# Kernel tuning notes

Hardware: AMD Instinct MI355X
Metric: run time of the kernel (lower is better)

## Reference

```python
import jax, jax.numpy as jnp
import numpy as np

EPROJS = 1024
DUNITS = 1024
AHEADS = 4
DK = 512
DV = 512
ACONV_CHANS = 128
ACONV_FILTS = 100
B = 16
T = 2048


def setup_inputs() -> dict:
    key = jax.random.key(0)
    ks = jax.random.split(key, 16)
    s = 0.02
    inp = {}
    inp["enc_hs_pad"] = jax.random.normal(ks[0], (B, T, EPROJS), jnp.float32)
    # lengths in [T//2, T] so no batch element is fully padded
    inp["enc_hs_len"] = jnp.sort(jax.random.randint(ks[1], (B,), T // 2, T + 1))
    inp["dec_z"] = jax.random.normal(ks[2], (B, DUNITS), jnp.float32)
    # per-head parameters, stacked on leading head axis where shapes match
    inp["Wq"] = jax.random.normal(ks[3], (AHEADS, DK, DUNITS), jnp.float32) * s
    inp["bq"] = jnp.zeros((AHEADS, DK), jnp.float32)
    inp["Wk"] = jax.random.normal(ks[4], (AHEADS, DK, EPROJS), jnp.float32) * s
    inp["Wv"] = jax.random.normal(ks[5], (AHEADS, DV, EPROJS), jnp.float32) * s
    inp["g_w"] = jax.random.normal(ks[6], (AHEADS, DK), jnp.float32) * s
    inp["g_b"] = jnp.zeros((AHEADS,), jnp.float32)
    inp["Watt"] = jax.random.normal(ks[7], (AHEADS, DK, ACONV_CHANS), jnp.float32) * s
    # conv kernels have DIFFERENT widths per head: 2*afilts+1, afilts = ACONV_FILTS*(h+1)//AHEADS
    for h in range(AHEADS):
        af = ACONV_FILTS * (h + 1) // AHEADS
        inp[f"conv_w_{h}"] = jax.random.normal(ks[8 + h], (ACONV_CHANS, 1, 2 * af + 1), jnp.float32) * s
    inp["Wo"] = jax.random.normal(ks[12], (EPROJS, AHEADS * DV), jnp.float32) * s
    return inp


def reference(enc_hs_pad, enc_hs_len, dec_z, Wq, bq, Wk, Wv, g_w, g_b, Watt,
              conv_w_0, conv_w_1, conv_w_2, conv_w_3, Wo):
    conv_ws = [conv_w_0, conv_w_1, conv_w_2, conv_w_3]
    Bb, Tt, _ = enc_hs_pad.shape
    scaling = jnp.float32(1.0) / jnp.sqrt(jnp.float32(DK))
    pos = jnp.arange(Tt)[None, :]                                   # (1,T)
    pad_mask = pos >= enc_hs_len[:, None]                           # (B,T) True at padding
    # att_prev=None path: uniform attention over valid frames (same for all heads)
    att_prev = (~pad_mask).astype(jnp.float32) / enc_hs_len[:, None].astype(jnp.float32)

    K = jnp.einsum('bte,hke->hbtk', enc_hs_pad, Wk)                 # pre_compute_k
    V = jnp.einsum('bte,hve->hbtv', enc_hs_pad, Wv)                 # pre_compute_v
    Q = jnp.einsum('bd,hkd->hbk', dec_z, Wq) + bq[:, None, :]       # mlp_q per head

    x = att_prev[:, None, :]                                        # (B,1,T) NCH
    cs, ws = [], []
    for h in range(AHEADS):  # heads have distinct conv widths -> structural loop
        wk = conv_ws[h]                                             # (C,1,2*af+1)
        af = (wk.shape[-1] - 1) // 2
        conv = jax.lax.conv_general_dilated(
            x, wk, window_strides=(1,), padding=[(af, af)],
            dimension_numbers=('NCH', 'OIH', 'NCH'))                # (B,C,T)
        att_feat = jnp.einsum('bct,kc->btk', conv, Watt[h])         # mlp_att
        e = jnp.einsum('btk,k->bt', jnp.tanh(K[h] + att_feat + Q[h][:, None, :]), g_w[h]) + g_b[h]
        e = jnp.where(pad_mask, -jnp.inf, e)
        w = jax.nn.softmax(scaling * e, axis=1)                     # (B,T)
        ws.append(w)
        cs.append(jnp.einsum('btv,bt->bv', V[h], w))                # weighted sum
    c = jnp.concatenate(cs, axis=1) @ Wo.T                          # (B,eprojs)
    return c, jnp.stack(ws)                                         # (B,eprojs), (H,B,T)
```

## Files before the change

### kernel.cpp

```cpp
#include <hip/hip_runtime.h>

#define EPROJS 1024
#define DUNITS 1024
#define AHEADS 4
#define DK 512
#define DV 512
#define CCH 128
#define BB 16
#define TT 2048

typedef __attribute__((ext_vector_type(8))) short bf16x8;
typedef __attribute__((ext_vector_type(4))) float f32x4;

static __device__ __forceinline__ short f2bf(float x) {
  unsigned u = __float_as_uint(x);
  unsigned r = u + 0x7fffu + ((u >> 16) & 1u);
  return (short)(r >> 16);
}
static __device__ __forceinline__ float bf2f(short x) {
  return __uint_as_float(((unsigned)(unsigned short)x) << 16);
}

static __device__ __forceinline__ float fast_tanh(float x) {
  float e2 = __expf(2.0f * x);
  return 1.0f - 2.0f / (e2 + 1.0f);
}

__global__ __launch_bounds__(256) void cvt_kernel(const float* __restrict__ in,
                                                  short* __restrict__ out, int n4) {
  int i = blockIdx.x * blockDim.x + threadIdx.x;
  if (i >= n4) return;
  float4 v = reinterpret_cast<const float4*>(in)[i];
  short4 o;
  o.x = f2bf(v.x); o.y = f2bf(v.y); o.z = f2bf(v.z); o.w = f2bf(v.w);
  reinterpret_cast<short4*>(out)[i] = o;
}

__global__ __launch_bounds__(256) void packB_kernel(const float* __restrict__ Wk,
                                                    const float* __restrict__ Watt,
                                                    short* __restrict__ Bp) {
  int idx = blockIdx.x * 256 + threadIdx.x;
  if (idx >= 294912) return;
  int lane = idx & 63; int t = idx >> 6;
  int nblk = t & 31; t >>= 5;
  int kkidx = t % 36; int h = t / 36;
  int col = nblk * 16 + (lane & 15);
  int k0 = kkidx * 32 + (lane >> 4) * 8;
  const float* src;
  if (k0 < 1024) src = Wk + ((size_t)(h * DK + col)) * EPROJS + k0;
  else           src = Watt + ((size_t)(h * DK + col)) * CCH + (k0 - 1024);
  float4 v0 = reinterpret_cast<const float4*>(src)[0];
  float4 v1 = reinterpret_cast<const float4*>(src)[1];
  short o[8] = { f2bf(v0.x), f2bf(v0.y), f2bf(v0.z), f2bf(v0.w),
                 f2bf(v1.x), f2bf(v1.y), f2bf(v1.z), f2bf(v1.w) };
  *reinterpret_cast<bf16x8*>(Bp + (size_t)idx * 8) = *reinterpret_cast<bf16x8*>(o);
}

__global__ __launch_bounds__(128) void prefix_kernel(const float* __restrict__ w0,
                                                     const float* __restrict__ w1,
                                                     const float* __restrict__ w2,
                                                     const float* __restrict__ w3,
                                                     float* __restrict__ S) {
  int h = blockIdx.x, c = threadIdx.x;
  const float* wk = (h == 0) ? w0 : (h == 1) ? w1 : (h == 2) ? w2 : w3;
  int af = (100 * (h + 1)) >> 2;
  int L = 2 * af + 1;
  float* Sh = S + h * 202 * 128;
  float s = 0.f;
  Sh[c] = 0.f;
  for (int t = 0; t < L; ++t) { s += wk[c * L + t]; Sh[(t + 1) * 128 + c] = s; }
}

__global__ __launch_bounds__(256) void q_kernel(const float* __restrict__ dec,
                                                const float* __restrict__ Wq,
                                                const float* __restrict__ bq,
                                                float* __restrict__ Qb) {
  int wid = (blockIdx.x * blockDim.x + threadIdx.x) >> 6;
  int lane = threadIdx.x & 63;
  int k = wid & (DK - 1); int hb = wid >> 9; int b = hb & (BB - 1); int h = hb >> 4;
  const float4* d4 = reinterpret_cast<const float4*>(dec + b * DUNITS);
  const float4* w4 = reinterpret_cast<const float4*>(Wq + (size_t)(h * DK + k) * DUNITS);
  float s = 0.f;
#pragma unroll
  for (int j = 0; j < 4; ++j) {
    float4 a = d4[j * 64 + lane], w = w4[j * 64 + lane];
    s += a.x * w.x + a.y * w.y + a.z * w.z + a.w * w.w;
  }
#pragma unroll
  for (int off = 32; off; off >>= 1) s += __shfl_xor(s, off);
  if (lane == 0) Qb[wid] = s + bq[h * DK + k];
}

__global__ __launch_bounds__(512, 3) void e_kernel(const short* __restrict__ encb,
                                                   const short* __restrict__ Bp,
                                                   const float* __restrict__ S,
                                                   const float* __restrict__ Qb,
                                                   const float* __restrict__ gw,
                                                   const float* __restrict__ gb,
                                                   const int* __restrict__ lens,
                                                   float* __restrict__ ebuf) {
  __shared__ short At[2][64 * 128];
  __shared__ short Ac[64 * 128];
  __shared__ float epart[8][64];

  int bid = blockIdx.x;
  int h = bid >> 9; int rem = bid & 511; int b = rem >> 5; int t0 = (rem & 31) << 6;
  int tid = threadIdx.x; int w = tid >> 6; int l = tid & 63;
  int lrow = l & 15, lhi = l >> 4;
  int len = lens[b];
  float invlen = 1.0f / (float)len;
  int af = (100 * (h + 1)) >> 2;

  const short* encB = encb + ((size_t)(b * TT + t0)) * EPROJS;
  const short* BpH = Bp + (size_t)h * 36 * 32 * 64 * 8;

  int srow = tid >> 3;
  int sc = tid & 7;
  int wo0 = srow * 128 + ((sc ^ (srow & 7)) << 3);
  int wo1 = srow * 128 + (((sc + 8) ^ (srow & 7)) << 3);
  const short* sbase = encB + (size_t)srow * EPROJS + sc * 8;

  int rx = lrow & 7;

  bf16x8 s0 = *reinterpret_cast<const bf16x8*>(sbase);
  bf16x8 s1 = *reinterpret_cast<const bf16x8*>(sbase + 64);

  const float* Sh = S + h * 202 * 128;
  for (int idx = tid; idx < 64 * 128; idx += 512) {
    int r = idx >> 7, c = idx & 127;
    int t = t0 + r;
    int lo = af - t; if (lo < 0) lo = 0;
    int hi = af - t + len - 1; if (hi > 2 * af) hi = 2 * af;
    float v = 0.f;
    if (hi >= lo) v = (Sh[(hi + 1) * 128 + c] - Sh[lo * 128 + c]) * invlen;
    Ac[r * 128 + (((c >> 3) ^ (r & 7)) << 3) + (c & 7)] = f2bf(v);
  }

  f32x4 acc[4][4] = {};

  bf16x8 bnext[4];
#pragma unroll
  for (int n = 0; n < 4; ++n)
    bnext[n] = *reinterpret_cast<const bf16x8*>(BpH + (((size_t)32 * 32 + (w * 4 + n)) * 64 + l) * 8);

  __syncthreads();

#pragma unroll
  for (int kk = 0; kk < 4; ++kk) {
    bf16x8 bcur[4];
#pragma unroll
    for (int n = 0; n < 4; ++n) bcur[n] = bnext[n];
    int nk = (kk < 3) ? (33 + kk) : 0;
#pragma unroll
    for (int n = 0; n < 4; ++n)
      bnext[n] = *reinterpret_cast<const bf16x8*>(BpH + (((size_t)nk * 32 + (w * 4 + n)) * 64 + l) * 8);
    bf16x8 afr[4];
    int x = (kk * 4 + lhi) ^ rx;
#pragma unroll
    for (int m = 0; m < 4; ++m)
      afr[m] = *reinterpret_cast<const bf16x8*>(&Ac[(m * 16 + lrow) * 128 + x * 8]);
#pragma unroll
    for (int m = 0; m < 4; ++m)
#pragma unroll
      for (int n = 0; n < 4; ++n)
        acc[m][n] = __builtin_amdgcn_mfma_f32_16x16x32_bf16(afr[m], bcur[n], acc[m][n], 0, 0, 0);
  }

  *reinterpret_cast<bf16x8*>(&At[0][wo0]) = s0;
  *reinterpret_cast<bf16x8*>(&At[0][wo1]) = s1;

  for (int tl = 0; tl < 8; ++tl) {
    int buf = tl & 1;
    if (tl < 7) {
      s0 = *reinterpret_cast<const bf16x8*>(sbase + (tl + 1) * 128);
      s1 = *reinterpret_cast<const bf16x8*>(sbase + (tl + 1) * 128 + 64);
    }
    __syncthreads();
#pragma unroll
    for (int kk = 0; kk < 4; ++kk) {
      bf16x8 bcur[4];
#pragma unroll
      for (int n = 0; n < 4; ++n) bcur[n] = bnext[n];
      int nk = tl * 4 + kk + 1;
      if (nk < 32) {
#pragma unroll
        for (int n = 0; n < 4; ++n)
          bnext[n] = *reinterpret_cast<const bf16x8*>(BpH + (((size_t)nk * 32 + (w * 4 + n)) * 64 + l) * 8);
      }
      bf16x8 afr[4];
      int x = (kk * 4 + lhi) ^ rx;
#pragma unroll
      for (int m = 0; m < 4; ++m)
        afr[m] = *reinterpret_cast<const bf16x8*>(&At[buf][(m * 16 + lrow) * 128 + x * 8]);
#pragma unroll
      for (int m = 0; m < 4; ++m)
#pragma unroll
        for (int n = 0; n < 4; ++n)
          acc[m][n] = __builtin_amdgcn_mfma_f32_16x16x32_bf16(afr[m], bcur[n], acc[m][n], 0, 0, 0);
    }
    if (tl < 7) {
      *reinterpret_cast<bf16x8*>(&At[buf ^ 1][wo0]) = s0;
      *reinterpret_cast<bf16x8*>(&At[buf ^ 1][wo1]) = s1;
    }
  }

  float part[4][4];
#pragma unroll
  for (int m = 0; m < 4; ++m)
#pragma unroll
    for (int r = 0; r < 4; ++r) part[m][r] = 0.f;

#pragma unroll
  for (int n = 0; n < 4; ++n) {
    int col = w * 64 + n * 16 + lrow;
    float q = Qb[(h * BB + b) * DK + col];
    float g = gw[h * DK + col];
#pragma unroll
    for (int m = 0; m < 4; ++m)
#pragma unroll
      for (int r = 0; r < 4; ++r)
        part[m][r] += fast_tanh(acc[m][n][r] + q) * g;
  }
#pragma unroll
  for (int off = 1; off < 16; off <<= 1)
#pragma unroll
    for (int m = 0; m < 4; ++m)
#pragma unroll
      for (int r = 0; r < 4; ++r) part[m][r] += __shfl_xor(part[m][r], off);

  if (lrow == 0) {
#pragma unroll
    for (int m = 0; m < 4; ++m)
#pragma unroll
      for (int r = 0; r < 4; ++r) epart[w][m * 16 + lhi * 4 + r] = part[m][r];
  }
  __syncthreads();
  if (tid < 64) {
    float s = gb[h];
#pragma unroll
    for (int ww = 0; ww < 8; ++ww) s += epart[ww][tid];
    ebuf[(size_t)(h * BB + b) * TT + t0 + tid] = s;
  }
}

__global__ __launch_bounds__(256) void softmax_kernel(const float* __restrict__ ebuf,
                                                      const int* __restrict__ lens,
                                                      float* __restrict__ wout) {
  int hb = blockIdx.x; int b = hb & (BB - 1);
  int tid = threadIdx.x;
  int len = lens[b];
  const float scaling = 0.04419417382415922f;
  const float* er = ebuf + (size_t)hb * TT;
  float vals[8];
  float mx = -1e30f;
#pragma unroll
  for (int j = 0; j < 8; ++j) {
    int t = j * 256 + tid;
    float v = (t < len) ? scaling * er[t] : -1e30f;
    vals[j] = v; mx = fmaxf(mx, v);
  }
  __shared__ float red[256];
  red[tid] = mx; __syncthreads();
  for (int s2 = 128; s2; s2 >>= 1) { if (tid < s2) red[tid] = fmaxf(red[tid], red[tid + s2]); __syncthreads(); }
  mx = red[0]; __syncthreads();
  float sum = 0.f;
#pragma unroll
  for (int j = 0; j < 8; ++j) {
    int t = j * 256 + tid;
    vals[j] = (t < len) ? __expf(vals[j] - mx) : 0.f;
    sum += vals[j];
  }
  red[tid] = sum; __syncthreads();
  for (int s2 = 128; s2; s2 >>= 1) { if (tid < s2) red[tid] += red[tid + s2]; __syncthreads(); }
  float inv = 1.f / red[0];
#pragma unroll
  for (int j = 0; j < 8; ++j)
    wout[(size_t)hb * TT + j * 256 + tid] = vals[j] * inv;
}

__global__ __launch_bounds__(256) void zero_kernel(float* __restrict__ p, int n) {
  int i = blockIdx.x * blockDim.x + threadIdx.x;
  if (i < n) p[i] = 0.f;
}

__global__ __launch_bounds__(256) void ctx_kernel(const short* __restrict__ encb,
                                                  const float* __restrict__ wout,
                                                  float* __restrict__ ctx) {
  int bid = blockIdx.x;
  int tc = bid & 7; int ec = (bid >> 3) & 3; int b = bid >> 5;
  int tid = threadIdx.x;
  int ecol = ec * 256 + tid;
  int t0 = tc * 256;
  __shared__ float wls[4][256];
#pragma unroll
  for (int h = 0; h < 4; ++h) wls[h][tid] = wout[(size_t)(h * BB + b) * TT + t0 + tid];
  __syncthreads();
  float a0 = 0.f, a1 = 0.f, a2 = 0.f, a3 = 0.f;
  const short* ep = encb + ((size_t)(b * TT + t0)) * EPROJS + ecol;
  for (int t2 = 0; t2 < 256; ++t2) {
    float v = bf2f(ep[(size_t)t2 * EPROJS]);
    a0 += wls[0][t2] * v; a1 += wls[1][t2] * v; a2 += wls[2][t2] * v; a3 += wls[3][t2] * v;
  }
  atomicAdd(&ctx[(0 * BB + b) * EPROJS + ecol], a0);
  atomicAdd(&ctx[(1 * BB + b) * EPROJS + ecol], a1);
  atomicAdd(&ctx[(2 * BB + b) * EPROJS + ecol], a2);
  atomicAdd(&ctx[(3 * BB + b) * EPROJS + ecol], a3);
}

__global__ __launch_bounds__(256) void cv_kernel(const float* __restrict__ ctx,
                                                 const float* __restrict__ Wv,
                                                 float* __restrict__ cvb) {
  int wid = (blockIdx.x * blockDim.x + threadIdx.x) >> 6;
  int lane = threadIdx.x & 63;
  int v = wid & (DV - 1); int h = wid >> 9;
  const float4* w4 = reinterpret_cast<const float4*>(Wv + (size_t)(h * DV + v) * EPROJS);
  float acc[BB];
#pragma unroll
  for (int b = 0; b < BB; ++b) acc[b] = 0.f;
#pragma unroll
  for (int j = 0; j < 4; ++j) {
    float4 ww = w4[j * 64 + lane];
#pragma unroll
    for (int b = 0; b < BB; ++b) {
      float4 a = reinterpret_cast<const float4*>(ctx + (size_t)(h * BB + b) * EPROJS)[j * 64 + lane];
      acc[b] += a.x * ww.x + a.y * ww.y + a.z * ww.z + a.w * ww.w;
    }
  }
#pragma unroll
  for (int off = 32; off; off >>= 1)
#pragma unroll
    for (int b = 0; b < BB; ++b) acc[b] += __shfl_xor(acc[b], off);
  if (lane == 0) {
#pragma unroll
    for (int b = 0; b < BB; ++b) cvb[b * 2048 + h * DV + v] = acc[b];
  }
}

__global__ __launch_bounds__(256) void out_kernel(const float* __restrict__ cvb,
                                                  const float* __restrict__ Wo,
                                                  float* __restrict__ outc) {
  int p = (blockIdx.x * blockDim.x + threadIdx.x) >> 6;
  int lane = threadIdx.x & 63;
  const float4* w4 = reinterpret_cast<const float4*>(Wo + (size_t)p * 2048);
  float acc[BB];
#pragma unroll
  for (int b = 0; b < BB; ++b) acc[b] = 0.f;
#pragma unroll
  for (int j = 0; j < 8; ++j) {
    float4 ww = w4[j * 64 + lane];
#pragma unroll
    for (int b = 0; b < BB; ++b) {
      float4 a = reinterpret_cast<const float4*>(cvb + (size_t)b * 2048)[j * 64 + lane];
      acc[b] += a.x * ww.x + a.y * ww.y + a.z * ww.z + a.w * ww.w;
    }
  }
#pragma unroll
  for (int off = 32; off; off >>= 1)
#pragma unroll
    for (int b = 0; b < BB; ++b) acc[b] += __shfl_xor(acc[b], off);
  if (lane == 0) {
#pragma unroll
    for (int b = 0; b < BB; ++b) outc[b * 1024 + p] = acc[b];
  }
}

extern "C" void kernel_launch(void* const* d_in, const int* in_sizes, int n_in,
                              void* d_out, int out_size, void* d_ws, size_t ws_size,
                              hipStream_t stream) {
  const float* enc  = (const float*)d_in[0];
  const int*   lens = (const int*)d_in[1];
  const float* dec  = (const float*)d_in[2];
  const float* Wq   = (const float*)d_in[3];
  const float* bq   = (const float*)d_in[4];
  const float* Wk   = (const float*)d_in[5];
  const float* Wv   = (const float*)d_in[6];
  const float* gw   = (const float*)d_in[7];
  const float* gb   = (const float*)d_in[8];
  const float* Watt = (const float*)d_in[9];
  const float* cw0  = (const float*)d_in[10];
  const float* cw1  = (const float*)d_in[11];
  const float* cw2  = (const float*)d_in[12];
  const float* cw3  = (const float*)d_in[13];
  const float* Wo   = (const float*)d_in[14];
  float* out = (float*)d_out;

  char* ws = (char*)d_ws;
  short* Bp    = (short*)(ws);
  float* S     = (float*)(ws + 4718592);
  float* Qb    = (float*)(ws + 5132288);
  float* ebuf  = (float*)(ws + 5263360);
  float* ctx   = (float*)(ws + 5787648);
  float* cvb   = (float*)(ws + 6049792);
  short* encb  = (short*)(ws + 6291456);

  float* wsout = out + 16384;

  cvt_kernel<<<32768, 256, 0, stream>>>(enc, encb, 8388608);
  packB_kernel<<<1152, 256, 0, stream>>>(Wk, Watt, Bp);
  prefix_kernel<<<4, 128, 0, stream>>>(cw0, cw1, cw2, cw3, S);
  q_kernel<<<8192, 256, 0, stream>>>(dec, Wq, bq, Qb);
  zero_kernel<<<256, 256, 0, stream>>>(ctx, 65536);
  e_kernel<<<2048, 512, 0, stream>>>(encb, Bp, S, Qb, gw, gb, lens, ebuf);
  softmax_kernel<<<64, 256, 0, stream>>>(ebuf, lens, wsout);
  ctx_kernel<<<512, 256, 0, stream>>>(encb, wsout, ctx);
  cv_kernel<<<512, 256, 0, stream>>>(ctx, Wv, cvb);
  out_kernel<<<256, 256, 0, stream>>>(cvb, Wo, out);
}
```

Measured before the change: 356.5 us.

## Split e_kernel over DK halves with 256-thread blocks and partial-sum softmax

The energy kernel now splits the 512-wide key dimension across two blocks of 256 threads each, doubling the grid. Each block writes a partial energy buffer, and the softmax adds the two halves. The conv-feature A tile is now built in registers as a ninth K-tile staged through the same double-buffered LDS path instead of a separate Ac buffer. B-fragments are prefetched four k-steps ahead in a register ring. This cuts LDS use and aims at better occupancy and load balance, but every block reloads the encoder tile twice as often and the energy buffer doubles. The g_b bias is no longer added; it is a per-head constant that softmax cancels, but the term is gone.

```diff
diff --git a/kernel.cpp b/kernel.cpp
--- a/kernel.cpp
+++ b/kernel.cpp
@@ -91,20 +91,21 @@
   if (lane == 0) Qb[wid] = s + bq[h * DK + k];
 }
 
-__global__ __launch_bounds__(512, 3) void e_kernel(const short* __restrict__ encb,
-                                                   const short* __restrict__ Bp,
-                                                   const float* __restrict__ S,
-                                                   const float* __restrict__ Qb,
-                                                   const float* __restrict__ gw,
-                                                   const float* __restrict__ gb,
-                                                   const int* __restrict__ lens,
-                                                   float* __restrict__ ebuf) {
+__global__ __launch_bounds__(256) void e_kernel(const short* __restrict__ encb,
+                                                const short* __restrict__ Bp,
+                                                const float* __restrict__ S,
+                                                const float* __restrict__ Qb,
+                                                const float* __restrict__ gw,
+                                                const int* __restrict__ lens,
+                                                float* __restrict__ ebuf2) {
   __shared__ short At[2][64 * 128];
-  __shared__ short Ac[64 * 128];
-  __shared__ float epart[8][64];
+  __shared__ float epart[4][64];
 
   int bid = blockIdx.x;
-  int h = bid >> 9; int rem = bid & 511; int b = rem >> 5; int t0 = (rem & 31) << 6;
+  int ch = bid & 1;
+  int t0 = ((bid >> 1) & 31) << 6;
+  int b  = (bid >> 6) & 15;
+  int h  = bid >> 10;
   int tid = threadIdx.x; int w = tid >> 6; int l = tid & 63;
   int lrow = l & 15, lhi = l >> 4;
   int len = lens[b];
@@ -112,95 +113,93 @@
   int af = (100 * (h + 1)) >> 2;
 
   const short* encB = encb + ((size_t)(b * TT + t0)) * EPROJS;
-  const short* BpH = Bp + (size_t)h * 36 * 32 * 64 * 8;
-
-  int srow = tid >> 3;
-  int sc = tid & 7;
-  int wo0 = srow * 128 + ((sc ^ (srow & 7)) << 3);
-  int wo1 = srow * 128 + (((sc + 8) ^ (srow & 7)) << 3);
-  const short* sbase = encB + (size_t)srow * EPROJS + sc * 8;
-
+  const short* pbase = Bp + (size_t)h * 589824 + ch * 8192 + w * 2048 + l * 8;
+
+  int srow = tid >> 2;
+  int sc4 = (tid & 3) * 4;
+  const short* sbase = encB + (size_t)srow * EPROJS + sc4 * 8;
+  int wo0 = srow * 128 + (((sc4 + 0) ^ (srow & 7)) << 3);
+  int wo1 = srow * 128 + (((sc4 + 1) ^ (srow & 7)) << 3);
+  int wo2 = srow * 128 + (((sc4 + 2) ^ (srow & 7)) << 3);
+  int wo3 = srow * 128 + (((sc4 + 3) ^ (srow & 7)) << 3);
   int rx = lrow & 7;
 
+  bf16x8 Bq[4][4];
+#pragma unroll
+  for (int kk = 0; kk < 4; ++kk)
+#pragma unroll
+    for (int n = 0; n < 4; ++n)
+      Bq[kk][n] = *reinterpret_cast<const bf16x8*>(pbase + kk * 16384 + n * 512);
+
   bf16x8 s0 = *reinterpret_cast<const bf16x8*>(sbase);
-  bf16x8 s1 = *reinterpret_cast<const bf16x8*>(sbase + 64);
-
-  const float* Sh = S + h * 202 * 128;
-  for (int idx = tid; idx < 64 * 128; idx += 512) {
-    int r = idx >> 7, c = idx & 127;
-    int t = t0 + r;
-    int lo = af - t; if (lo < 0) lo = 0;
-    int hi = af - t + len - 1; if (hi > 2 * af) hi = 2 * af;
-    float v = 0.f;
-    if (hi >= lo) v = (Sh[(hi + 1) * 128 + c] - Sh[lo * 128 + c]) * invlen;
-    Ac[r * 128 + (((c >> 3) ^ (r & 7)) << 3) + (c & 7)] = f2bf(v);
-  }
+  bf16x8 s1 = *reinterpret_cast<const bf16x8*>(sbase + 8);
+  bf16x8 s2 = *reinterpret_cast<const bf16x8*>(sbase + 16);
+  bf16x8 s3 = *reinterpret_cast<const bf16x8*>(sbase + 24);
 
   f32x4 acc[4][4] = {};
-
-  bf16x8 bnext[4];
-#pragma unroll
-  for (int n = 0; n < 4; ++n)
-    bnext[n] = *reinterpret_cast<const bf16x8*>(BpH + (((size_t)32 * 32 + (w * 4 + n)) * 64 + l) * 8);
-
-  __syncthreads();
-
-#pragma unroll
-  for (int kk = 0; kk < 4; ++kk) {
-    bf16x8 bcur[4];
-#pragma unroll
-    for (int n = 0; n < 4; ++n) bcur[n] = bnext[n];
-    int nk = (kk < 3) ? (33 + kk) : 0;
-#pragma unroll
-    for (int n = 0; n < 4; ++n)
-      bnext[n] = *reinterpret_cast<const bf16x8*>(BpH + (((size_t)nk * 32 + (w * 4 + n)) * 64 + l) * 8);
-    bf16x8 afr[4];
-    int x = (kk * 4 + lhi) ^ rx;
-#pragma unroll
-    for (int m = 0; m < 4; ++m)
-      afr[m] = *reinterpret_cast<const bf16x8*>(&Ac[(m * 16 + lrow) * 128 + x * 8]);
-#pragma unroll
-    for (int m = 0; m < 4; ++m)
-#pragma unroll
-      for (int n = 0; n < 4; ++n)
-        acc[m][n] = __builtin_amdgcn_mfma_f32_16x16x32_bf16(afr[m], bcur[n], acc[m][n], 0, 0, 0);
-  }
 
   *reinterpret_cast<bf16x8*>(&At[0][wo0]) = s0;
   *reinterpret_cast<bf16x8*>(&At[0][wo1]) = s1;
-
-  for (int tl = 0; tl < 8; ++tl) {
-    int buf = tl & 1;
+  *reinterpret_cast<bf16x8*>(&At[0][wo2]) = s2;
+  *reinterpret_cast<bf16x8*>(&At[0][wo3]) = s3;
+
+  const float* Sh = S + h * 202 * 128;
+
+#pragma unroll
+  for (int tl = 0; tl < 9; ++tl) {
     if (tl < 7) {
-      s0 = *reinterpret_cast<const bf16x8*>(sbase + (tl + 1) * 128);
-      s1 = *reinterpret_cast<const bf16x8*>(sbase + (tl + 1) * 128 + 64);
+      const short* sp = sbase + (tl + 1) * 128;
+      s0 = *reinterpret_cast<const bf16x8*>(sp);
+      s1 = *reinterpret_cast<const bf16x8*>(sp + 8);
+      s2 = *reinterpret_cast<const bf16x8*>(sp + 16);
+      s3 = *reinterpret_cast<const bf16x8*>(sp + 24);
+    } else if (tl == 7) {
+      int t = t0 + srow;
+      int lo = af - t; if (lo < 0) lo = 0;
+      int hi = af - t + len - 1; if (hi > 2 * af) hi = 2 * af;
+      bool any = (hi >= lo);
+      const float* Plo = Sh + lo * 128;
+      const float* Phi = Sh + (hi + 1) * 128;
+#pragma unroll
+      for (int j = 0; j < 4; ++j) {
+        short o[8];
+#pragma unroll
+        for (int e = 0; e < 8; ++e) {
+          int c = (sc4 + j) * 8 + e;
+          float v = any ? (Phi[c] - Plo[c]) * invlen : 0.f;
+          o[e] = f2bf(v);
+        }
+        bf16x8 pk = *reinterpret_cast<bf16x8*>(o);
+        if (j == 0) s0 = pk; else if (j == 1) s1 = pk; else if (j == 2) s2 = pk; else s3 = pk;
+      }
     }
     __syncthreads();
 #pragma unroll
     for (int kk = 0; kk < 4; ++kk) {
-      bf16x8 bcur[4];
-#pragma unroll
-      for (int n = 0; n < 4; ++n) bcur[n] = bnext[n];
-      int nk = tl * 4 + kk + 1;
-      if (nk < 32) {
+      bf16x8 afr[4];
+      int x = ((kk * 4 + lhi) ^ rx) << 3;
+#pragma unroll
+      for (int m = 0; m < 4; ++m)
+        afr[m] = *reinterpret_cast<const bf16x8*>(&At[tl & 1][(m * 16 + lrow) * 128 + x]);
+#pragma unroll
+      for (int m = 0; m < 4; ++m)
 #pragma unroll
         for (int n = 0; n < 4; ++n)
-          bnext[n] = *reinterpret_cast<const bf16x8*>(BpH + (((size_t)nk * 32 + (w * 4 + n)) * 64 + l) * 8);
+          acc[m][n] = __builtin_amdgcn_mfma_f32_16x16x32_bf16(afr[m], Bq[kk][n], acc[m][n], 0, 0, 0);
+      int bi = tl * 4 + kk + 4;
+      if (bi < 36) {
+        const short* bp = pbase + (size_t)bi * 16384;
+#pragma unroll
+        for (int n = 0; n < 4; ++n)
+          Bq[kk][n] = *reinterpret_cast<const bf16x8*>(bp + n * 512);
       }
-      bf16x8 afr[4];
-      int x = (kk * 4 + lhi) ^ rx;
-#pragma unroll
-      for (int m = 0; m < 4; ++m)
-        afr[m] = *reinterpret_cast<const bf16x8*>(&At[buf][(m * 16 + lrow) * 128 + x * 8]);
-#pragma unroll
-      for (int m = 0; m < 4; ++m)
-#pragma unroll
-        for (int n = 0; n < 4; ++n)
-          acc[m][n] = __builtin_amdgcn_mfma_f32_16x16x32_bf16(afr[m], bcur[n], acc[m][n], 0, 0, 0);
     }
-    if (tl < 7) {
-      *reinterpret_cast<bf16x8*>(&At[buf ^ 1][wo0]) = s0;
-      *reinterpret_cast<bf16x8*>(&At[buf ^ 1][wo1]) = s1;
+    if (tl < 8) {
+      int nb = (tl + 1) & 1;
+      *reinterpret_cast<bf16x8*>(&At[nb][wo0]) = s0;
+      *reinterpret_cast<bf16x8*>(&At[nb][wo1]) = s1;
+      *reinterpret_cast<bf16x8*>(&At[nb][wo2]) = s2;
+      *reinterpret_cast<bf16x8*>(&At[nb][wo3]) = s3;
     }
   }
 
@@ -212,7 +211,7 @@
 
 #pragma unroll
   for (int n = 0; n < 4; ++n) {
-    int col = w * 64 + n * 16 + lrow;
+    int col = ch * 256 + w * 64 + n * 16 + lrow;
     float q = Qb[(h * BB + b) * DK + col];
     float g = gw[h * DK + col];
 #pragma unroll
@@ -236,27 +235,28 @@
   }
   __syncthreads();
   if (tid < 64) {
-    float s = gb[h];
-#pragma unroll
-    for (int ww = 0; ww < 8; ++ww) s += epart[ww][tid];
-    ebuf[(size_t)(h * BB + b) * TT + t0 + tid] = s;
-  }
-}
-
-__global__ __launch_bounds__(256) void softmax_kernel(const float* __restrict__ ebuf,
+    float s = 0.f;
+#pragma unroll
+    for (int ww = 0; ww < 4; ++ww) s += epart[ww][tid];
+    ebuf2[(size_t)((ch * 64) + h * BB + b) * TT + t0 + tid] = s;
+  }
+}
+
+__global__ __launch_bounds__(256) void softmax_kernel(const float* __restrict__ ebuf2,
                                                       const int* __restrict__ lens,
                                                       float* __restrict__ wout) {
   int hb = blockIdx.x; int b = hb & (BB - 1);
   int tid = threadIdx.x;
   int len = lens[b];
   const float scaling = 0.04419417382415922f;
-  const float* er = ebuf + (size_t)hb * TT;
+  const float* e0 = ebuf2 + (size_t)hb * TT;
+  const float* e1 = ebuf2 + (size_t)(64 + hb) * TT;
   float vals[8];
   float mx = -1e30f;
 #pragma unroll
   for (int j = 0; j < 8; ++j) {
     int t = j * 256 + tid;
-    float v = (t < len) ? scaling * er[t] : -1e30f;
+    float v = (t < len) ? scaling * (e0[t] + e1[t]) : -1e30f;
     vals[j] = v; mx = fmaxf(mx, v);
   }
   __shared__ float red[256];
@@ -375,7 +375,6 @@
   const float* Wk   = (const float*)d_in[5];
   const float* Wv   = (const float*)d_in[6];
   const float* gw   = (const float*)d_in[7];
-  const float* gb   = (const float*)d_in[8];
   const float* Watt = (const float*)d_in[9];
   const float* cw0  = (const float*)d_in[10];
   const float* cw1  = (const float*)d_in[11];
@@ -388,10 +387,10 @@
   short* Bp    = (short*)(ws);
   float* S     = (float*)(ws + 4718592);
   float* Qb    = (float*)(ws + 5132288);
-  float* ebuf  = (float*)(ws + 5263360);
-  float* ctx   = (float*)(ws + 5787648);
-  float* cvb   = (float*)(ws + 6049792);
-  short* encb  = (short*)(ws + 6291456);
+  float* ebuf2 = (float*)(ws + 5263360);
+  float* ctx   = (float*)(ws + 6311936);
+  float* cvb   = (float*)(ws + 6574080);
+  short* encb  = (short*)(ws + 6815744);
 
   float* wsout = out + 16384;
 
@@ -400,8 +399,8 @@
   prefix_kernel<<<4, 128, 0, stream>>>(cw0, cw1, cw2, cw3, S);
   q_kernel<<<8192, 256, 0, stream>>>(dec, Wq, bq, Qb);
   zero_kernel<<<256, 256, 0, stream>>>(ctx, 65536);
-  e_kernel<<<2048, 512, 0, stream>>>(encb, Bp, S, Qb, gw, gb, lens, ebuf);
-  softmax_kernel<<<64, 256, 0, stream>>>(ebuf, lens, wsout);
+  e_kernel<<<4096, 256, 0, stream>>>(encb, Bp, S, Qb, gw, lens, ebuf2);
+  softmax_kernel<<<64, 256, 0, stream>>>(ebuf2, lens, wsout);
   ctx_kernel<<<512, 256, 0, stream>>>(encb, wsout, ctx);
   cv_kernel<<<512, 256, 0, stream>>>(ctx, Wv, cvb);
   out_kernel<<<256, 256, 0, stream>>>(cvb, Wo, out);
```

Measured after the change: 417.4 us. +17.1%, slower.

## Fold att-conv tile into e_kernel K pipeline, remap blocks per XCD, drop gb

Applied to the files above, without the earlier changes.

The separate Ac shared buffer and its prologue GEMM pass are removed. The conv-feature tile is now computed as a ninth stage of the double-buffered At pipeline, which cuts LDS use and overlaps that work with the MFMA loop. Block IDs are remapped so the four heads that share the same (b, t0) encoder tile land on the same XCD, aiming for better L2 reuse. The constant g_b bias is dropped because softmax is invariant to a per-row shift. The workspace offsets for ctx, cvb and encb are also moved.

```diff
diff --git a/kernel.cpp b/kernel.cpp
--- a/kernel.cpp
+++ b/kernel.cpp
@@ -96,15 +96,17 @@
                                                    const float* __restrict__ S,
                                                    const float* __restrict__ Qb,
                                                    const float* __restrict__ gw,
-                                                   const float* __restrict__ gb,
                                                    const int* __restrict__ lens,
                                                    float* __restrict__ ebuf) {
   __shared__ short At[2][64 * 128];
-  __shared__ short Ac[64 * 128];
   __shared__ float epart[8][64];
 
   int bid = blockIdx.x;
-  int h = bid >> 9; int rem = bid & 511; int b = rem >> 5; int t0 = (rem & 31) << 6;
+  int xcd = bid & 7; int q = bid >> 3;
+  int h = q & 3; int gq = q >> 2;
+  int g = xcd + (gq << 3);
+  int b = g >> 5; int t0 = (g & 31) << 6;
+
   int tid = threadIdx.x; int w = tid >> 6; int l = tid & 63;
   int lrow = l & 15, lhi = l >> 4;
   int len = lens[b];
@@ -112,68 +114,51 @@
   int af = (100 * (h + 1)) >> 2;
 
   const short* encB = encb + ((size_t)(b * TT + t0)) * EPROJS;
-  const short* BpH = Bp + (size_t)h * 36 * 32 * 64 * 8;
+  const short* BpH = Bp + (size_t)h * 589824;
 
   int srow = tid >> 3;
   int sc = tid & 7;
   int wo0 = srow * 128 + ((sc ^ (srow & 7)) << 3);
   int wo1 = srow * 128 + (((sc + 8) ^ (srow & 7)) << 3);
   const short* sbase = encB + (size_t)srow * EPROJS + sc * 8;
-
   int rx = lrow & 7;
+
+  bf16x8 bnext[4];
+#pragma unroll
+  for (int n = 0; n < 4; ++n)
+    bnext[n] = *reinterpret_cast<const bf16x8*>(BpH + (w * 4 + n) * 512 + l * 8);
 
   bf16x8 s0 = *reinterpret_cast<const bf16x8*>(sbase);
   bf16x8 s1 = *reinterpret_cast<const bf16x8*>(sbase + 64);
 
-  const float* Sh = S + h * 202 * 128;
-  for (int idx = tid; idx < 64 * 128; idx += 512) {
-    int r = idx >> 7, c = idx & 127;
-    int t = t0 + r;
-    int lo = af - t; if (lo < 0) lo = 0;
-    int hi = af - t + len - 1; if (hi > 2 * af) hi = 2 * af;
-    float v = 0.f;
-    if (hi >= lo) v = (Sh[(hi + 1) * 128 + c] - Sh[lo * 128 + c]) * invlen;
-    Ac[r * 128 + (((c >> 3) ^ (r & 7)) << 3) + (c & 7)] = f2bf(v);
-  }
-
   f32x4 acc[4][4] = {};
-
-  bf16x8 bnext[4];
-#pragma unroll
-  for (int n = 0; n < 4; ++n)
-    bnext[n] = *reinterpret_cast<const bf16x8*>(BpH + (((size_t)32 * 32 + (w * 4 + n)) * 64 + l) * 8);
-
-  __syncthreads();
-
-#pragma unroll
-  for (int kk = 0; kk < 4; ++kk) {
-    bf16x8 bcur[4];
-#pragma unroll
-    for (int n = 0; n < 4; ++n) bcur[n] = bnext[n];
-    int nk = (kk < 3) ? (33 + kk) : 0;
-#pragma unroll
-    for (int n = 0; n < 4; ++n)
-      bnext[n] = *reinterpret_cast<const bf16x8*>(BpH + (((size_t)nk * 32 + (w * 4 + n)) * 64 + l) * 8);
-    bf16x8 afr[4];
-    int x = (kk * 4 + lhi) ^ rx;
-#pragma unroll
-    for (int m = 0; m < 4; ++m)
-      afr[m] = *reinterpret_cast<const bf16x8*>(&Ac[(m * 16 + lrow) * 128 + x * 8]);
-#pragma unroll
-    for (int m = 0; m < 4; ++m)
-#pragma unroll
-      for (int n = 0; n < 4; ++n)
-        acc[m][n] = __builtin_amdgcn_mfma_f32_16x16x32_bf16(afr[m], bcur[n], acc[m][n], 0, 0, 0);
-  }
 
   *reinterpret_cast<bf16x8*>(&At[0][wo0]) = s0;
   *reinterpret_cast<bf16x8*>(&At[0][wo1]) = s1;
 
-  for (int tl = 0; tl < 8; ++tl) {
-    int buf = tl & 1;
+  const float* Sh = S + h * 202 * 128;
+
+  for (int tl = 0; tl < 9; ++tl) {
     if (tl < 7) {
       s0 = *reinterpret_cast<const bf16x8*>(sbase + (tl + 1) * 128);
       s1 = *reinterpret_cast<const bf16x8*>(sbase + (tl + 1) * 128 + 64);
+    } else if (tl == 7) {
+      int t = t0 + srow;
+      int lo = af - t; if (lo < 0) lo = 0;
+      int hi = af - t + len - 1; if (hi > 2 * af) hi = 2 * af;
+      bool any = (hi >= lo);
+      const float* Plo = Sh + lo * 128;
+      const float* Phi = Sh + (hi + 1) * 128;
+      short o0[8], o1[8];
+#pragma unroll
+      for (int e = 0; e < 8; ++e) {
+        int c = sc * 8 + e;
+        float v0 = any ? (Phi[c] - Plo[c]) * invlen : 0.f;
+        float v1 = any ? (Phi[c + 64] - Plo[c + 64]) * invlen : 0.f;
+        o0[e] = f2bf(v0); o1[e] = f2bf(v1);
+      }
+      s0 = *reinterpret_cast<bf16x8*>(o0);
+      s1 = *reinterpret_cast<bf16x8*>(o1);
     }
     __syncthreads();
 #pragma unroll
@@ -182,25 +167,27 @@
 #pragma unroll
       for (int n = 0; n < 4; ++n) bcur[n] = bnext[n];
       int nk = tl * 4 + kk + 1;
-      if (nk < 32) {
+      if (nk < 36) {
+        const short* bp = BpH + (size_t)nk * 16384 + l * 8;
 #pragma unroll
         for (int n = 0; n < 4; ++n)
-          bnext[n] = *reinterpret_cast<const bf16x8*>(BpH + (((size_t)nk * 32 + (w * 4 + n)) * 64 + l) * 8);
+          bnext[n] = *reinterpret_cast<const bf16x8*>(bp + (w * 4 + n) * 512);
       }
       bf16x8 afr[4];
-      int x = (kk * 4 + lhi) ^ rx;
+      int x = ((kk * 4 + lhi) ^ rx) << 3;
 #pragma unroll
       for (int m = 0; m < 4; ++m)
-        afr[m] = *reinterpret_cast<const bf16x8*>(&At[buf][(m * 16 + lrow) * 128 + x * 8]);
+        afr[m] = *reinterpret_cast<const bf16x8*>(&At[tl & 1][(m * 16 + lrow) * 128 + x]);
 #pragma unroll
       for (int m = 0; m < 4; ++m)
 #pragma unroll
         for (int n = 0; n < 4; ++n)
           acc[m][n] = __builtin_amdgcn_mfma_f32_16x16x32_bf16(afr[m], bcur[n], acc[m][n], 0, 0, 0);
     }
-    if (tl < 7) {
-      *reinterpret_cast<bf16x8*>(&At[buf ^ 1][wo0]) = s0;
-      *reinterpret_cast<bf16x8*>(&At[buf ^ 1][wo1]) = s1;
+    if (tl < 8) {
+      int nb = (tl + 1) & 1;
+      *reinterpret_cast<bf16x8*>(&At[nb][wo0]) = s0;
+      *reinterpret_cast<bf16x8*>(&At[nb][wo1]) = s1;
     }
   }
 
@@ -213,13 +200,13 @@
 #pragma unroll
   for (int n = 0; n < 4; ++n) {
     int col = w * 64 + n * 16 + lrow;
-    float q = Qb[(h * BB + b) * DK + col];
-    float g = gw[h * DK + col];
+    float qv = Qb[(h * BB + b) * DK + col];
+    float gv = gw[h * DK + col];
 #pragma unroll
     for (int m = 0; m < 4; ++m)
 #pragma unroll
       for (int r = 0; r < 4; ++r)
-        part[m][r] += fast_tanh(acc[m][n][r] + q) * g;
+        part[m][r] += fast_tanh(acc[m][n][r] + qv) * gv;
   }
 #pragma unroll
   for (int off = 1; off < 16; off <<= 1)
@@ -236,7 +223,7 @@
   }
   __syncthreads();
   if (tid < 64) {
-    float s = gb[h];
+    float s = 0.f;
 #pragma unroll
     for (int ww = 0; ww < 8; ++ww) s += epart[ww][tid];
     ebuf[(size_t)(h * BB + b) * TT + t0 + tid] = s;
@@ -375,7 +362,6 @@
   const float* Wk   = (const float*)d_in[5];
   const float* Wv   = (const float*)d_in[6];
   const float* gw   = (const float*)d_in[7];
-  const float* gb   = (const float*)d_in[8];
   const float* Watt = (const float*)d_in[9];
   const float* cw0  = (const float*)d_in[10];
   const float* cw1  = (const float*)d_in[11];
@@ -389,9 +375,9 @@
   float* S     = (float*)(ws + 4718592);
   float* Qb    = (float*)(ws + 5132288);
   float* ebuf  = (float*)(ws + 5263360);
-  float* ctx   = (float*)(ws + 5787648);
-  float* cvb   = (float*)(ws + 6049792);
-  short* encb  = (short*)(ws + 6291456);
+  float* ctx   = (float*)(ws + 6311936);
+  float* cvb   = (float*)(ws + 6574080);
+  short* encb  = (short*)(ws + 6815744);
 
   float* wsout = out + 16384;
 
@@ -400,7 +386,7 @@
   prefix_kernel<<<4, 128, 0, stream>>>(cw0, cw1, cw2, cw3, S);
   q_kernel<<<8192, 256, 0, stream>>>(dec, Wq, bq, Qb);
   zero_kernel<<<256, 256, 0, stream>>>(ctx, 65536);
-  e_kernel<<<2048, 512, 0, stream>>>(encb, Bp, S, Qb, gw, gb, lens, ebuf);
+  e_kernel<<<2048, 512, 0, stream>>>(encb, Bp, S, Qb, gw, lens, ebuf);
   softmax_kernel<<<64, 256, 0, stream>>>(ebuf, lens, wsout);
   ctx_kernel<<<512, 256, 0, stream>>>(encb, wsout, ctx);
   cv_kernel<<<512, 256, 0, stream>>>(ctx, Wv, cvb);
```

Result: slower. 364.0 us (+2.1%).
